# Kernel optimization log

Measured on AMD Instinct MI355X. Metric: run time of the kernel, lower is better.

The kernel has to match this reference:

```python
import jax, jax.numpy as jnp
import numpy as np

OUT, IN = 11008, 4096
B, S = 8, 32


def setup_inputs() -> dict:
    key = jax.random.key(0)
    k_x, k_w, k_s, k_b = jax.random.split(key, 4)
    x = jax.random.normal(k_x, (B, S, IN), dtype=jnp.float32).astype(jnp.float16)
    # int8 weight storage (symmetric quant range [-128, 127])
    w_int8 = jax.random.randint(k_w, (OUT, IN), -128, 128, dtype=jnp.int32).astype(jnp.int8)
    # per-output-channel scale, small positive values typical of int8 quant
    scale = jax.random.uniform(k_s, (OUT,), dtype=jnp.float32) * 0.01 + 1e-4
    bias = (jax.random.normal(k_b, (OUT,), dtype=jnp.float32) * 0.02).astype(jnp.float16)
    return {"x": x, "w_int8": w_int8, "scale": scale, "bias": bias}


def reference(x, w_int8, scale, bias):
    # w_fp[o, i] = int8_weight[o, i] * scale[o]   (on-the-fly dequant)
    w = w_int8.astype(jnp.float32) * scale[:, None]          # [OUT, IN] fp32
    # F.linear: out = x @ w.T + bias, computed in fp32
    out = jnp.einsum('bsi,oi->bso', x.astype(jnp.float32), w) + bias.astype(jnp.float32)
    return out.astype(x.dtype)                                # cast back to x.dtype (fp16)
```

## Files before the change

kernel.cpp:

```cpp
#include <hip/hip_runtime.h>
#include <hip/hip_bf16.h>
#include <stdint.h>

typedef __attribute__((ext_vector_type(8))) __bf16 bf16x8;
typedef __attribute__((ext_vector_type(4))) float f32x4;

constexpr int K_DIM = 4096;
constexpr int N_DIM = 11008;
constexpr int M_DIM = 256;
constexpr int TM = 256;
constexpr int TN = 64;
constexpr int BK = 64;
constexpr int NT = 512;
constexpr int KT_ALL = K_DIM / BK;
constexpr int KSPLIT = 3;
constexpr int WTILE = TN * BK;

__device__ __forceinline__ void gload_lds16(const __bf16* gptr, __bf16* lptr) {
  __builtin_amdgcn_global_load_lds(
      (const __attribute__((address_space(1))) uint32_t*)gptr,
      (__attribute__((address_space(3))) uint32_t*)lptr, 16, 0, 0);
}

__device__ __forceinline__ bf16x8 cvt8f(const float4 u0, const float4 u1) {
  bf16x8 v;
  v[0] = (__bf16)u0.x; v[1] = (__bf16)u0.y; v[2] = (__bf16)u0.z; v[3] = (__bf16)u0.w;
  v[4] = (__bf16)u1.x; v[5] = (__bf16)u1.y; v[6] = (__bf16)u1.z; v[7] = (__bf16)u1.w;
  return v;
}
__device__ __forceinline__ bf16x8 cvt8i(const int4 a, const int4 b) {
  bf16x8 v;
  v[0] = (__bf16)(float)a.x; v[1] = (__bf16)(float)a.y;
  v[2] = (__bf16)(float)a.z; v[3] = (__bf16)(float)a.w;
  v[4] = (__bf16)(float)b.x; v[5] = (__bf16)(float)b.y;
  v[6] = (__bf16)(float)b.z; v[7] = (__bf16)(float)b.w;
  return v;
}

__global__ void cvt_x_kernel(const float* __restrict__ x, __bf16* __restrict__ ws) {
  const int i = (blockIdx.x * 256 + threadIdx.x) * 8;
  const float4 u0 = ((const float4*)(x + i))[0];
  const float4 u1 = ((const float4*)(x + i))[1];
  *(bf16x8*)(ws + i) = cvt8f(u0, u1);
}

__global__ void pack_w_kernel(const int* __restrict__ w, int8_t* __restrict__ wp) {
  const int j = blockIdx.x * 256 + threadIdx.x;
  const int e = j * 32;
  const int tile = e >> 12;
  const int o = e & 4095;
  const int wrow = o >> 6;
  const int col0 = o & 63;
  const int nb = tile >> 6, kt = tile & 63;
  const int4* src = (const int4*)(w + (int64_t)(nb * 64 + wrow) * K_DIM + kt * 64 + col0);
  int pk[8];
#pragma unroll
  for (int q = 0; q < 8; ++q) {
    const int4 a = src[q];
    pk[q] = (a.x & 0xFF) | ((a.y & 0xFF) << 8) | ((a.z & 0xFF) << 16) | (a.w << 24);
  }
  int4* dst = (int4*)(wp + (size_t)e);
  dst[0] = make_int4(pk[0], pk[1], pk[2], pk[3]);
  dst[1] = make_int4(pk[4], pk[5], pk[6], pk[7]);
}

template<bool A_WS, bool W_PK>
__global__ __launch_bounds__(NT, 4) void int8_linear_kernel(
    const float* __restrict__ x,
    const __bf16* __restrict__ xws,
    const int*   __restrict__ w,
    const int8_t* __restrict__ wp,
    const float* __restrict__ scale,
    const float* __restrict__ bias,
    float*       __restrict__ out)
{
  __shared__ __bf16 As[2][TM * BK];
  __shared__ __bf16 Wsh[2][TN * BK];

  const int tid  = threadIdx.x;
  const int lane = tid & 63;
  const int wv   = tid >> 6;
  const int quad = lane >> 4;
  const int l16  = lane & 15;
  const int m_base = (wv >> 1) * 64;
  const int wn     = wv & 1;
  const int nb     = blockIdx.x;
  const int n_base = nb * TN;
  const int kc     = blockIdx.y;

  const int t0 = (kc * KT_ALL) / KSPLIT;
  const int t1 = ((kc + 1) * KT_ALL) / KSPLIT;
  const int ntile = t1 - t0;

  const int wrow   = tid >> 3;
  const int wchunk = tid & 7;
  const int wslot  = wchunk ^ (wrow & 7);

  f32x4 acc[4][2];
#pragma unroll
  for (int i = 0; i < 4; ++i)
#pragma unroll
    for (int j = 0; j < 2; ++j) acc[i][j] = (f32x4){0.f, 0.f, 0.f, 0.f};

  uint2 pw;
  int4  wi0, wi1;
  auto wload = [&](int t) {
    if (W_PK) {
      pw = *(const uint2*)(wp + (size_t)(nb * KT_ALL + t0 + t) * WTILE + tid * 8);
    } else {
      const int4* p = (const int4*)(w + (int64_t)(n_base + wrow) * K_DIM +
                                    (t0 + t) * BK + wchunk * 8);
      wi0 = p[0]; wi1 = p[1];
    }
  };
  auto commitW = [&](__bf16* wbuf) {
    bf16x8 v;
    if (W_PK) {
#pragma unroll
      for (int e = 0; e < 4; ++e)
        v[e] = (__bf16)(float)(int)(int8_t)((pw.x >> (8 * e)) & 0xFF);
#pragma unroll
      for (int e = 0; e < 4; ++e)
        v[4 + e] = (__bf16)(float)(int)(int8_t)((pw.y >> (8 * e)) & 0xFF);
    } else {
      v = cvt8i(wi0, wi1);
    }
    *(bf16x8*)(wbuf + wrow * BK + wslot * 8) = v;
  };
  auto a_stage = [&](int t, __bf16* abuf) {
    const int kt = t0 + t;
    if (A_WS) {
#pragma unroll
      for (int j = 0; j < 4; ++j) {
        const int c = j * 512 + tid;
        const int row = c >> 3;
        const int k8 = (c & 7) ^ (row & 7);
        gload_lds16(xws + (int64_t)row * K_DIM + kt * BK + k8 * 8, abuf + c * 8);
      }
    } else {
#pragma unroll
      for (int j = 0; j < 4; ++j) {
        const int c = j * 512 + tid;
        const int row = c >> 3;
        const int k8 = c & 7;
        const float* s = x + (int64_t)row * K_DIM + kt * BK + k8 * 8;
        const bf16x8 vv = cvt8f(((const float4*)s)[0], ((const float4*)s)[1]);
        *(bf16x8*)(abuf + row * BK + (k8 ^ (row & 7)) * 8) = vv;
      }
    }
  };
  auto compute = [&](const __bf16* abuf, const __bf16* wbuf) {
#pragma unroll
    for (int ks = 0; ks < 2; ++ks) {
      bf16x8 a[4], b[2];
#pragma unroll
      for (int mi = 0; mi < 4; ++mi) {
        const int m = m_base + mi * 16 + l16;
        const int slot = (ks * 4 + quad) ^ (m & 7);
        a[mi] = *(const bf16x8*)(abuf + m * BK + slot * 8);
      }
#pragma unroll
      for (int ni = 0; ni < 2; ++ni) {
        const int n = wn * 32 + ni * 16 + l16;
        const int slot = (ks * 4 + quad) ^ (n & 7);
        b[ni] = *(const bf16x8*)(wbuf + n * BK + slot * 8);
      }
#pragma unroll
      for (int mi = 0; mi < 4; ++mi)
#pragma unroll
        for (int ni = 0; ni < 2; ++ni)
          acc[mi][ni] = __builtin_amdgcn_mfma_f32_16x16x32_bf16(
              a[mi], b[ni], acc[mi][ni], 0, 0, 0);
    }
  };

  wload(0);
  commitW(Wsh[0]);
  a_stage(0, As[0]);
  __syncthreads();

  for (int t = 0; t < ntile; ++t) {
    const int nxt = (t + 1) & 1;
    const bool more = (t + 1 < ntile);
    if (more) { wload(t + 1); a_stage(t + 1, As[nxt]); }
    compute(As[t & 1], Wsh[t & 1]);
    if (more) commitW(Wsh[nxt]);
    __syncthreads();
  }

#pragma unroll
  for (int ni = 0; ni < 2; ++ni) {
    const int col = n_base + wn * 32 + ni * 16 + l16;
    const float sc = scale[col];
    const float bi = (kc == 0) ? bias[col] : 0.0f;
#pragma unroll
    for (int mi = 0; mi < 4; ++mi) {
      const int row0 = m_base + mi * 16 + quad * 4;
#pragma unroll
      for (int r = 0; r < 4; ++r)
        unsafeAtomicAdd(out + (int64_t)(row0 + r) * N_DIM + col,
                        acc[mi][ni][r] * sc + bi);
    }
  }
}

extern "C" void kernel_launch(void* const* d_in, const int* in_sizes, int n_in,
                              void* d_out, int out_size, void* d_ws, size_t ws_size,
                              hipStream_t stream) {
  const float* x     = (const float*)d_in[0];
  const int*   w     = (const int*)d_in[1];
  const float* scale = (const float*)d_in[2];
  const float* bias  = (const float*)d_in[3];
  float* out = (float*)d_out;

  const size_t xws_bytes = (size_t)M_DIM * K_DIM * sizeof(__bf16);
  const size_t wp_bytes  = (size_t)N_DIM * K_DIM;
  __bf16* xws = (__bf16*)d_ws;
  int8_t* wpp = (int8_t*)((char*)d_ws + xws_bytes);

  hipMemsetAsync(out, 0, (size_t)M_DIM * N_DIM * sizeof(float), stream);

  dim3 grid(N_DIM / TN, KSPLIT), block(NT);
  if (ws_size >= xws_bytes + wp_bytes) {
    cvt_x_kernel<<<M_DIM * K_DIM / 2048, 256, 0, stream>>>(x, xws);
    pack_w_kernel<<<(int)(((size_t)N_DIM * K_DIM / 32) / 256), 256, 0, stream>>>(w, wpp);
    int8_linear_kernel<true, true><<<grid, block, 0, stream>>>(
        x, xws, w, wpp, scale, bias, out);
  } else if (ws_size >= xws_bytes) {
    cvt_x_kernel<<<M_DIM * K_DIM / 2048, 256, 0, stream>>>(x, xws);
    int8_linear_kernel<true, false><<<grid, block, 0, stream>>>(
        x, xws, w, wpp, scale, bias, out);
  } else {
    int8_linear_kernel<false, false><<<grid, block, 0, stream>>>(
        x, xws, w, wpp, scale, bias, out);
  }
}
```

Baseline: 339.2 us.

## Retile int8 linear to 128x128 blocks with M split across grid z

```diff
diff --git a/kernel.cpp b/kernel.cpp
--- a/kernel.cpp
+++ b/kernel.cpp
@@ -8,12 +8,13 @@
 constexpr int K_DIM = 4096;
 constexpr int N_DIM = 11008;
 constexpr int M_DIM = 256;
-constexpr int TM = 256;
-constexpr int TN = 64;
+constexpr int TM = 128;
+constexpr int TN = 128;
 constexpr int BK = 64;
 constexpr int NT = 512;
 constexpr int KT_ALL = K_DIM / BK;
 constexpr int KSPLIT = 3;
+constexpr int NB = N_DIM / TN;
 constexpr int WTILE = TN * BK;
 
 __device__ __forceinline__ void gload_lds16(const __bf16* gptr, __bf16* lptr) {
@@ -46,20 +47,20 @@
 
 __global__ void pack_w_kernel(const int* __restrict__ w, int8_t* __restrict__ wp) {
   const int j = blockIdx.x * 256 + threadIdx.x;
-  const int e = j * 32;
-  const int tile = e >> 12;
-  const int o = e & 4095;
-  const int wrow = o >> 6;
+  const size_t e = (size_t)j * 32;
+  const int tile = (int)(e >> 13);
+  const int o = (int)(e & 8191);
+  const int row = o >> 6;
   const int col0 = o & 63;
   const int nb = tile >> 6, kt = tile & 63;
-  const int4* src = (const int4*)(w + (int64_t)(nb * 64 + wrow) * K_DIM + kt * 64 + col0);
+  const int4* src = (const int4*)(w + (int64_t)(nb * TN + row) * K_DIM + kt * BK + col0);
   int pk[8];
 #pragma unroll
   for (int q = 0; q < 8; ++q) {
     const int4 a = src[q];
     pk[q] = (a.x & 0xFF) | ((a.y & 0xFF) << 8) | ((a.z & 0xFF) << 16) | (a.w << 24);
   }
-  int4* dst = (int4*)(wp + (size_t)e);
+  int4* dst = (int4*)(wp + e);
   dst[0] = make_int4(pk[0], pk[1], pk[2], pk[3]);
   dst[1] = make_int4(pk[4], pk[5], pk[6], pk[7]);
 }
@@ -82,19 +83,19 @@
   const int wv   = tid >> 6;
   const int quad = lane >> 4;
   const int l16  = lane & 15;
-  const int m_base = (wv >> 1) * 64;
-  const int wn     = wv & 1;
+  const int m_base = (wv >> 2) * 64;
+  const int wn     = wv & 3;
   const int nb     = blockIdx.x;
   const int n_base = nb * TN;
   const int kc     = blockIdx.y;
+  const int mb     = blockIdx.z;
 
   const int t0 = (kc * KT_ALL) / KSPLIT;
   const int t1 = ((kc + 1) * KT_ALL) / KSPLIT;
   const int ntile = t1 - t0;
 
-  const int wrow   = tid >> 3;
-  const int wchunk = tid & 7;
-  const int wslot  = wchunk ^ (wrow & 7);
+  const int wrow = tid >> 2;
+  const int wc2  = tid & 3;
 
   f32x4 acc[4][2];
 #pragma unroll
@@ -102,48 +103,56 @@
 #pragma unroll
     for (int j = 0; j < 2; ++j) acc[i][j] = (f32x4){0.f, 0.f, 0.f, 0.f};
 
-  uint2 pw;
-  int4  wi0, wi1;
+  uint4 pw;
+  int4 wi[4];
   auto wload = [&](int t) {
     if (W_PK) {
-      pw = *(const uint2*)(wp + (size_t)(nb * KT_ALL + t0 + t) * WTILE + tid * 8);
+      pw = *(const uint4*)(wp + (size_t)(nb * KT_ALL + t0 + t) * WTILE + tid * 16);
     } else {
       const int4* p = (const int4*)(w + (int64_t)(n_base + wrow) * K_DIM +
-                                    (t0 + t) * BK + wchunk * 8);
-      wi0 = p[0]; wi1 = p[1];
+                                    (t0 + t) * BK + wc2 * 16);
+#pragma unroll
+      for (int q = 0; q < 4; ++q) wi[q] = p[q];
     }
   };
   auto commitW = [&](__bf16* wbuf) {
-    bf16x8 v;
-    if (W_PK) {
-#pragma unroll
-      for (int e = 0; e < 4; ++e)
-        v[e] = (__bf16)(float)(int)(int8_t)((pw.x >> (8 * e)) & 0xFF);
-#pragma unroll
-      for (int e = 0; e < 4; ++e)
-        v[4 + e] = (__bf16)(float)(int)(int8_t)((pw.y >> (8 * e)) & 0xFF);
-    } else {
-      v = cvt8i(wi0, wi1);
-    }
-    *(bf16x8*)(wbuf + wrow * BK + wslot * 8) = v;
+#pragma unroll
+    for (int h = 0; h < 2; ++h) {
+      bf16x8 v;
+      const uint32_t lo = h ? pw.z : pw.x;
+      const uint32_t hi = h ? pw.w : pw.y;
+      if (W_PK) {
+#pragma unroll
+        for (int e = 0; e < 4; ++e)
+          v[e] = (__bf16)(float)(int)(int8_t)((lo >> (8 * e)) & 0xFF);
+#pragma unroll
+        for (int e = 0; e < 4; ++e)
+          v[4 + e] = (__bf16)(float)(int)(int8_t)((hi >> (8 * e)) & 0xFF);
+      } else {
+        v = cvt8i(wi[h * 2], wi[h * 2 + 1]);
+      }
+      const int chunk = wc2 * 2 + h;
+      *(bf16x8*)(wbuf + wrow * BK + (chunk ^ (wrow & 7)) * 8) = v;
+    }
   };
   auto a_stage = [&](int t, __bf16* abuf) {
     const int kt = t0 + t;
     if (A_WS) {
 #pragma unroll
-      for (int j = 0; j < 4; ++j) {
+      for (int j = 0; j < 2; ++j) {
         const int c = j * 512 + tid;
         const int row = c >> 3;
         const int k8 = (c & 7) ^ (row & 7);
-        gload_lds16(xws + (int64_t)row * K_DIM + kt * BK + k8 * 8, abuf + c * 8);
+        gload_lds16(xws + (int64_t)(mb * TM + row) * K_DIM + kt * BK + k8 * 8,
+                    abuf + c * 8);
       }
     } else {
 #pragma unroll
-      for (int j = 0; j < 4; ++j) {
+      for (int j = 0; j < 2; ++j) {
         const int c = j * 512 + tid;
         const int row = c >> 3;
         const int k8 = c & 7;
-        const float* s = x + (int64_t)row * K_DIM + kt * BK + k8 * 8;
+        const float* s = x + (int64_t)(mb * TM + row) * K_DIM + kt * BK + k8 * 8;
         const bf16x8 vv = cvt8f(((const float4*)s)[0], ((const float4*)s)[1]);
         *(bf16x8*)(abuf + row * BK + (k8 ^ (row & 7)) * 8) = vv;
       }
@@ -195,7 +204,7 @@
     const float bi = (kc == 0) ? bias[col] : 0.0f;
 #pragma unroll
     for (int mi = 0; mi < 4; ++mi) {
-      const int row0 = m_base + mi * 16 + quad * 4;
+      const int row0 = mb * TM + m_base + mi * 16 + quad * 4;
 #pragma unroll
       for (int r = 0; r < 4; ++r)
         unsafeAtomicAdd(out + (int64_t)(row0 + r) * N_DIM + col,
@@ -220,7 +229,7 @@
 
   hipMemsetAsync(out, 0, (size_t)M_DIM * N_DIM * sizeof(float), stream);
 
-  dim3 grid(N_DIM / TN, KSPLIT), block(NT);
+  dim3 grid(NB, KSPLIT, M_DIM / TM), block(NT);
   if (ws_size >= xws_bytes + wp_bytes) {
     cvt_x_kernel<<<M_DIM * K_DIM / 2048, 256, 0, stream>>>(x, xws);
     pack_w_kernel<<<(int)(((size_t)N_DIM * K_DIM / 32) / 256), 256, 0, stream>>>(w, wpp);
```

After: 340.8 us. Within noise of the previous version (+0.5%).
